# Optimization experiments

Measured on AMD Instinct MI355X. Metric: run time of the kernel, lower is better.

Reference implementation:

```python
import jax, jax.numpy as jnp
import numpy as np

N, E, F, H, O = 50000, 800000, 256, 128, 64


def setup_inputs() -> dict:
    key = jax.random.key(0)
    ks = jax.random.split(key, 8)
    x = jax.random.normal(ks[0], (N, F), jnp.float32)
    edge_index = jax.random.randint(ks[1], (2, E), 0, N, jnp.int32)
    batch = jnp.zeros((N,), jnp.int32)  # single graph
    s = 0.05
    W0 = jax.random.normal(ks[2], (F, H), jnp.float32) * s
    W1 = jax.random.normal(ks[3], (H, H), jnp.float32) * s
    W2 = jax.random.normal(ks[4], (H, H), jnp.float32) * s
    Wlin = jax.random.normal(ks[5], (H, O), jnp.float32) * s
    b0 = jnp.zeros((H,), jnp.float32)
    b1 = jnp.zeros((H,), jnp.float32)
    b2 = jnp.zeros((H,), jnp.float32)
    blin = jnp.zeros((O,), jnp.float32)
    return {"x": x, "edge_index": edge_index, "batch": batch,
            "W0": W0, "b0": b0, "W1": W1, "b1": b1, "W2": W2, "b2": b2,
            "Wlin": Wlin, "blin": blin}


def _gcn_norm(edge_index, n, dtype):
    # GCNConv: add self-loops, symmetric normalization D^-1/2 (A+I) D^-1/2
    loop = jnp.arange(n, dtype=edge_index.dtype)
    src = jnp.concatenate([edge_index[0], loop])
    dst = jnp.concatenate([edge_index[1], loop])
    deg = jax.ops.segment_sum(jnp.ones_like(dst, dtype=dtype), dst, num_segments=n)
    dinv = jnp.where(deg > 0, jax.lax.rsqrt(deg), 0.0)
    norm = dinv[src] * dinv[dst]  # [E+N]
    return src, dst, norm


def _gcn_conv(h, src, dst, norm, b, n):
    # gather-transform-scatter: message = norm * h[src], aggregate at dst
    msg = h[src] * norm[:, None]
    return jax.ops.segment_sum(msg, dst, num_segments=n) + b


def reference(x, edge_index, batch, W0, b0, W1, b1, W2, b2, Wlin, blin):
    n = x.shape[0]
    src, dst, norm = _gcn_norm(edge_index, n, x.dtype)
    h = _gcn_conv(x @ W0, src, dst, norm, b0, n)   # no inter-layer activation in source
    h = _gcn_conv(h @ W1, src, dst, norm, b1, n)
    h = _gcn_conv(h @ W2, src, dst, norm, b2, n)
    # dropout p=0.2 is identity in eval mode
    h = h @ Wlin + blin
    out = jax.ops.segment_max(h, batch, num_segments=1)  # global_max_pool, single graph
    return out
```

## Files before the change

kernel.cpp:

```cpp
#include <hip/hip_runtime.h>
#include <math.h>


typedef __attribute__((ext_vector_type(8))) _Float16 f16x8;
typedef __attribute__((ext_vector_type(4))) _Float16 f16x4;
typedef __attribute__((ext_vector_type(4))) float f32x4;

__device__ __forceinline__ unsigned enc_f32(float f) {
    unsigned u = __float_as_uint(f);
    return (u & 0x80000000u) ? ~u : (u | 0x80000000u);
}
__device__ __forceinline__ float dec_f32(unsigned e) {
    return (e & 0x80000000u) ? __uint_as_float(e & 0x7fffffffu)
                             : __uint_as_float(~e);
}
#define ENC_NEG_INF 0x007FFFFFu

__global__ __launch_bounds__(256) void k_hist(const int* __restrict__ dst,
                                              int* __restrict__ T,
                                              int E, int NB, int chunk) {
    __shared__ int hist[512];
    for (int i = threadIdx.x; i < 512; i += 256) hist[i] = 0;
    __syncthreads();
    const int lo = blockIdx.x * chunk, hi = min(E, lo + chunk);
    for (int e = lo + threadIdx.x; e < hi; e += 256)
        atomicAdd(&hist[dst[e] >> 7], 1);
    __syncthreads();
    for (int b = threadIdx.x; b < NB; b += 256)
        T[b * 256 + blockIdx.x] = hist[b];
}

__global__ __launch_bounds__(1024) void k_scan1(const int* __restrict__ in,
                                                int* __restrict__ excl,
                                                int* __restrict__ bsums, int L) {
    __shared__ int sh[1024];
    int t = threadIdx.x;
    int i = blockIdx.x * 1024 + t;
    int v = (i < L) ? in[i] : 0;
    sh[t] = v;
    __syncthreads();
    for (int off = 1; off < 1024; off <<= 1) {
        int tv = (t >= off) ? sh[t - off] : 0;
        __syncthreads();
        sh[t] += tv;
        __syncthreads();
    }
    if (i < L) excl[i] = sh[t] - v;
    if (t == 1023) bsums[blockIdx.x] = sh[1023];
}

__global__ __launch_bounds__(1024) void k_scan2(const int* __restrict__ bsums,
                                                int* __restrict__ bofs, int nb) {
    __shared__ int sh[1024];
    int t = threadIdx.x;
    int v = (t < nb) ? bsums[t] : 0;
    sh[t] = v;
    __syncthreads();
    for (int off = 1; off < 1024; off <<= 1) {
        int tv = (t >= off) ? sh[t - off] : 0;
        __syncthreads();
        sh[t] += tv;
        __syncthreads();
    }
    if (t < nb) bofs[t] = sh[t] - v;
}

__global__ void k_scan3(int* __restrict__ arr, const int* __restrict__ bofs, int L) {
    int i = blockIdx.x * blockDim.x + threadIdx.x;
    if (i < L) arr[i] += bofs[i >> 10];
}

#define PBT 4096
__global__ __launch_bounds__(256) void k_part(const int* __restrict__ src,
                                              const int* __restrict__ dst,
                                              const int* __restrict__ T2,
                                              unsigned* __restrict__ eb,
                                              int E, int NB, int chunk) {
    __shared__ int hist[512], lexc[512], pos[512], wpos[512];
    __shared__ unsigned sorted[PBT];
    const int t = threadIdx.x;
    const int blk = blockIdx.x;
    const int lo = blk * chunk, hi = min(E, lo + chunk);
    for (int i = t; i < NB; i += 256) wpos[i] = T2[i * 256 + blk];
    __syncthreads();
    for (int tlo = lo; tlo < hi; tlo += PBT) {
        const int thi = min(hi, tlo + PBT);
        const int sz = thi - tlo;
        for (int i = t; i < 512; i += 256) hist[i] = 0;
        __syncthreads();
        for (int e = tlo + t; e < thi; e += 256)
            atomicAdd(&hist[dst[e] >> 7], 1);
        __syncthreads();
        const int i0 = t, i1 = t + 256;
        const int o0 = hist[i0], o1 = hist[i1];
        for (int off = 1; off < 512; off <<= 1) {
            int v0 = (i0 >= off) ? hist[i0 - off] : 0;
            int v1 = (i1 >= off) ? hist[i1 - off] : 0;
            __syncthreads();
            hist[i0] += v0;
            hist[i1] += v1;
            __syncthreads();
        }
        lexc[i0] = hist[i0] - o0; pos[i0] = hist[i0] - o0;
        lexc[i1] = hist[i1] - o1; pos[i1] = hist[i1] - o1;
        __syncthreads();
        for (int e = tlo + t; e < thi; e += 256) {
            int d = dst[e];
            int p = atomicAdd(&pos[d >> 7], 1);
            sorted[p] = ((unsigned)d << 16) | (unsigned)src[e];
        }
        __syncthreads();
        for (int i = t; i < sz; i += 256) {
            unsigned x = sorted[i];
            int b = (int)(x >> 23);
            eb[wpos[b] + (i - lexc[b])] = x;
        }
        __syncthreads();
        wpos[i0] += o0;
        wpos[i1] += o1;
        __syncthreads();
    }
}

#define PCT 6144
__global__ __launch_bounds__(256) void k_build(const unsigned* __restrict__ eb,
                                               const int* __restrict__ T2,
                                               unsigned short* __restrict__ csr,
                                               int* __restrict__ rofs,
                                               float* __restrict__ dinv,
                                               int N, int E, int NB) {
    __shared__ int hist[128], lofs[128], pos[128];
    __shared__ unsigned short ssrc[PCT];
    const int t = threadIdx.x;
    const int b = blockIdx.x;
    const int glo = T2[b * 256];
    const int ghi = (b + 1 < NB) ? T2[(b + 1) * 256] : E;
    const int sz = ghi - glo;
    if (t < 128) hist[t] = 0;
    __syncthreads();
    for (int i = t; i < sz; i += 256)
        atomicAdd(&hist[(eb[glo + i] >> 16) & 127], 1);
    __syncthreads();
    const int o = (t < 128) ? hist[t] : 0;
    for (int off = 1; off < 128; off <<= 1) {
        int v = (t < 128 && t >= off) ? hist[t - off] : 0;
        __syncthreads();
        if (t < 128) hist[t] += v;
        __syncthreads();
    }
    if (t < 128) {
        int ex = hist[t] - o;
        lofs[t] = ex;
        pos[t] = ex;
        int d = b * 128 + t;
        if (d < N) {
            rofs[d] = glo + ex;
            dinv[d] = rsqrtf((float)(o + 1));
        }
    }
    __syncthreads();
    if (sz <= PCT) {
        for (int i = t; i < sz; i += 256) {
            unsigned x = eb[glo + i];
            int p = atomicAdd(&pos[(x >> 16) & 127], 1);
            ssrc[p] = (unsigned short)(x & 0xFFFFu);
        }
        __syncthreads();
        for (int i = t; i < sz; i += 256) csr[glo + i] = ssrc[i];
    } else {
        for (int i = t; i < sz; i += 256) {
            unsigned x = eb[glo + i];
            int p = atomicAdd(&pos[(x >> 16) & 127], 1);
            csr[glo + p] = (unsigned short)(x & 0xFFFFu);
        }
    }
    if (b == 0 && t == 0) rofs[N] = E;
}

template <int PACK>
__global__ __launch_bounds__(256) void k_mm2(const float* __restrict__ A,
                                             const float* __restrict__ B,
                                             float* __restrict__ C,
                                             _Float16* __restrict__ Wp) {
    __shared__ float Bs[128 * 64];
    __shared__ float As[4 * 128];
    const int tid = threadIdx.x;
    const int r0 = blockIdx.x * 4;
#pragma unroll
    for (int it = 0; it < 8; ++it) {
        int f = tid + it * 256;
        *(float4*)&Bs[f * 4] = *(const float4*)&B[(size_t)f * 4];
    }
    if (tid < 128)
        *(float4*)&As[tid * 4] = *(const float4*)&A[(size_t)r0 * 128 + tid * 4];
    __syncthreads();
    const int n = tid & 63;
    const int rh = tid >> 6;
    float a0 = 0.f, a1 = 0.f, a2 = 0.f, a3 = 0.f;
#pragma unroll
    for (int k = 0; k < 128; k += 4) {
        a0 = fmaf(As[rh * 128 + k + 0], Bs[(k + 0) * 64 + n], a0);
        a1 = fmaf(As[rh * 128 + k + 1], Bs[(k + 1) * 64 + n], a1);
        a2 = fmaf(As[rh * 128 + k + 2], Bs[(k + 2) * 64 + n], a2);
        a3 = fmaf(As[rh * 128 + k + 3], Bs[(k + 3) * 64 + n], a3);
    }
    float acc = (a0 + a1) + (a2 + a3);
    const int kk = r0 + rh;
    if (PACK) {
        int j = kk & 7;
        int l = ((kk >> 3) & 3) * 16 + (n & 15);
        int q = kk >> 5;
        int c = n >> 4;
        Wp[((size_t)(c * 8 + q) * 64 + l) * 8 + j] = (_Float16)acc;
    } else {
        C[(size_t)kk * 64 + n] = acc;
    }
}

__global__ __launch_bounds__(256) void k_cvec(const float* __restrict__ b0,
                                              const float* __restrict__ b1,
                                              const float* __restrict__ b2,
                                              const float* __restrict__ blin,
                                              const float* __restrict__ P,
                                              const float* __restrict__ Q,
                                              const float* __restrict__ Wl,
                                              float* __restrict__ cv) {
    __shared__ int nzf;
    if (threadIdx.x == 0) nzf = 0;
    __syncthreads();
    const int v = threadIdx.x >> 6;
    const int n = threadIdx.x & 63;
    if (v < 3) {
        const float* bb = (v == 0) ? b0 : (v == 1) ? b1 : b2;
        const float* M = (v == 0) ? P : (v == 1) ? Q : Wl;
        float a0 = 0.f, a1 = 0.f, a2 = 0.f, a3 = 0.f;
#pragma unroll
        for (int k = 0; k < 128; k += 4) {
            a0 = fmaf(bb[k + 0], M[(k + 0) * 64 + n], a0);
            a1 = fmaf(bb[k + 1], M[(k + 1) * 64 + n], a1);
            a2 = fmaf(bb[k + 2], M[(k + 2) * 64 + n], a2);
            a3 = fmaf(bb[k + 3], M[(k + 3) * 64 + n], a3);
        }
        float c = (a0 + a1) + (a2 + a3);
        if (v == 2) c += blin[n];
        cv[v * 64 + n] = c;
        if (v < 2 && c != 0.f) atomicOr(&nzf, 1);
    }
    __syncthreads();
    if (threadIdx.x == 0) cv[192] = nzf ? 1.f : 0.f;
}

__global__ __launch_bounds__(256) void k_u1(const float* __restrict__ dinv,
                                            const int* __restrict__ rofs,
                                            const unsigned short* __restrict__ csr,
                                            const float* __restrict__ cv,
                                            float* __restrict__ u1,
                                            float* __restrict__ w1, int N) {
    int d = blockIdx.x * 256 + threadIdx.x;
    if (d >= N) return;
    if (cv[192] == 0.f) { u1[d] = 0.f; w1[d] = 0.f; return; }
    float s = 0.f;
    const int beg = rofs[d], end = rofs[d + 1];
    for (int e = beg; e < end; ++e) s += dinv[csr[e]];
    float di = dinv[d];
    float u = di * (s + di);
    u1[d] = u;
    w1[d] = di * u;
}

__global__ __launch_bounds__(256) void k_u2(const float* __restrict__ dinv,
                                            const int* __restrict__ rofs,
                                            const unsigned short* __restrict__ csr,
                                            const float* __restrict__ cv,
                                            const float* __restrict__ w1,
                                            float* __restrict__ u2, int N) {
    int d = blockIdx.x * 256 + threadIdx.x;
    if (d >= N) return;
    if (cv[192] == 0.f) { u2[d] = 0.f; return; }
    float s = 0.f;
    const int beg = rofs[d], end = rofs[d + 1];
    for (int e = beg; e < end; ++e) s += w1[csr[e]];
    u2[d] = dinv[d] * (s + w1[d]);
}

template <int K, int M>
__global__ __launch_bounds__(256, 4) void k_gemm(const void* __restrict__ Av,
                                                 const _Float16* __restrict__ Wp,
                                                 const float* __restrict__ sc,
                                                 _Float16* __restrict__ out,
                                                 int N) {
    constexpr int KB = (K > 128) ? 128 : K;
    constexpr int NQ = K / KB;
    constexpr int NK = KB / 32;
    constexpr int KG = KB / 8;
    constexpr int CT = M / 32;
    constexpr int RT = 3;
    __shared__ _Float16 As[96 * KB];
    const int tid = threadIdx.x;
    const int lane = tid & 63;
    const int wave = tid >> 6;
    const int wrow = wave >> 1;
    const int wcol = wave & 1;
    const int R0 = blockIdx.x * 96;

    f32x4 acc[RT][CT];
#pragma unroll
    for (int rt = 0; rt < RT; ++rt)
#pragma unroll
        for (int ct = 0; ct < CT; ++ct) acc[rt][ct] = (f32x4){0.f, 0.f, 0.f, 0.f};

    for (int q = 0; q < NQ; ++q) {
        if (q) __syncthreads();
        {
            const float* A = (const float*)Av;
#pragma unroll
            for (int it = 0; it < (96 * KB) / (4 * 256); ++it) {
                int idx = tid + it * 256;
                int r = idx >> 5;
                int f4 = idx & 31;
                float4 g = {0.f, 0.f, 0.f, 0.f};
                if (R0 + r < N) g = *(const float4*)&A[(size_t)(R0 + r) * K + q * KB + f4 * 4];
                int kg = f4 >> 1, sub = f4 & 1;
                f16x4 h;
                h[0] = (_Float16)g.x; h[1] = (_Float16)g.y;
                h[2] = (_Float16)g.z; h[3] = (_Float16)g.w;
                *(f16x4*)&As[(r >> 4) * (KG * 128) + kg * 128 + (((r & 15) ^ kg) * 8) + sub * 4] = h;
            }
        }
        __syncthreads();
#pragma unroll
        for (int qq = 0; qq < NK; ++qq) {
            const int kk = q * NK + qq;
            const int kgq = qq * 4 + (lane >> 4);
            f16x8 af[RT], bf[CT];
#pragma unroll
            for (int ct = 0; ct < CT; ++ct) {
                int t = wcol * CT + ct;
                bf[ct] = *(const f16x8*)&Wp[((size_t)(t * (K / 32) + kk) * 64 + lane) * 8];
            }
#pragma unroll
            for (int rt = 0; rt < RT; ++rt) {
                int tr = wrow * RT + rt;
                af[rt] = *(const f16x8*)&As[tr * (KG * 128) + kgq * 128 + (((lane & 15) ^ kgq) * 8)];
            }
#pragma unroll
            for (int rt = 0; rt < RT; ++rt)
#pragma unroll
                for (int ct = 0; ct < CT; ++ct)
                    acc[rt][ct] = __builtin_amdgcn_mfma_f32_16x16x32_f16(af[rt], bf[ct], acc[rt][ct], 0, 0, 0);
        }
    }

    const int quad = lane >> 4;
#pragma unroll
    for (int rt = 0; rt < RT; ++rt)
#pragma unroll
        for (int reg = 0; reg < 4; ++reg) {
            int r = R0 + wrow * 48 + rt * 16 + quad * 4 + reg;
            if (r < N) {
                float s = sc[r];
#pragma unroll
                for (int ct = 0; ct < CT; ++ct) {
                    int c = wcol * (CT * 16) + ct * 16 + (lane & 15);
                    out[(size_t)r * M + c] = (_Float16)(acc[rt][ct][reg] * s);
                }
            }
        }
}

template <int FIN>
__global__ __launch_bounds__(256) void k_agg64(const _Float16* __restrict__ tmp,
                                               const float* __restrict__ dinv,
                                               const int* __restrict__ rofs,
                                               const unsigned short* __restrict__ csr,
                                               const float* __restrict__ u1,
                                               const float* __restrict__ u2,
                                               const float* __restrict__ cv,
                                               _Float16* __restrict__ out,
                                               float* __restrict__ bmax, int N) {
    __shared__ unsigned smax[64];
    const int tid = threadIdx.x;
    const int lane = tid & 63;
    const int wave = tid >> 6;
    const int d = blockIdx.x * 4 + wave;
    const int eh = lane >> 3;
    const int fl = lane & 7;
    if (FIN) {
        if (tid < 64) smax[tid] = ENC_NEG_INF;
        __syncthreads();
    }
    if (d < N) {
        const int beg = rofs[d], end = rofs[d + 1];
        float a[8];
#pragma unroll
        for (int j = 0; j < 8; ++j) a[j] = 0.f;
        f16x8 vd;
        if (eh == 7) vd = *(const f16x8*)&tmp[(size_t)d * 64 + fl * 8];
        for (int base = beg; base < end; base += 32) {
            f16x8 v[4];
            unsigned msk = 0;
#pragma unroll
            for (int i = 0; i < 4; ++i) {
                int idx = base + 8 * i + eh;
                if (idx < end) {
                    int s = csr[idx];
                    v[i] = *(const f16x8*)&tmp[(size_t)s * 64 + fl * 8];
                    msk |= 1u << i;
                }
            }
#pragma unroll
            for (int i = 0; i < 4; ++i)
                if (msk & (1u << i)) {
#pragma unroll
                    for (int j = 0; j < 8; ++j) a[j] += (float)v[i][j];
                }
        }
        if (eh == 7) {
#pragma unroll
            for (int j = 0; j < 8; ++j) a[j] += (float)vd[j];
        }
#pragma unroll
        for (int j = 0; j < 8; ++j) {
            a[j] += __shfl_xor(a[j], 8, 64);
            a[j] += __shfl_xor(a[j], 16, 64);
            a[j] += __shfl_xor(a[j], 32, 64);
        }
        if (FIN == 0) {
            if (eh == 0) {
                float di = dinv[d];
                float s2 = di * di;
                f16x8 o;
#pragma unroll
                for (int j = 0; j < 8; ++j) o[j] = (_Float16)(a[j] * s2);
                *(f16x8*)&out[(size_t)d * 64 + fl * 8] = o;
            }
        } else {
            if (eh == 0) {
                float di = dinv[d];
                float v1 = u1[d], v2 = u2[d];
#pragma unroll
                for (int j = 0; j < 8; ++j) {
                    int f = fl * 8 + j;
                    float z = fmaf(di, a[j],
                              fmaf(v2, cv[f], fmaf(v1, cv[64 + f], cv[128 + f])));
                    atomicMax(&smax[f], enc_f32(z));
                }
            }
        }
    }
    if (FIN) {
        __syncthreads();
        if (tid < 64) bmax[(size_t)blockIdx.x * 64 + tid] = dec_f32(smax[tid]);
    }
}

__global__ __launch_bounds__(256) void k_pool(const float* __restrict__ bmax,
                                              float* __restrict__ out, int nb) {
    __shared__ float sm[4];
    const int f = blockIdx.x;
    float m = -INFINITY;
    for (int b = threadIdx.x; b < nb; b += 256)
        m = fmaxf(m, bmax[(size_t)b * 64 + f]);
#pragma unroll
    for (int off = 1; off < 64; off <<= 1) m = fmaxf(m, __shfl_xor(m, off, 64));
    if ((threadIdx.x & 63) == 0) sm[threadIdx.x >> 6] = m;
    __syncthreads();
    if (threadIdx.x == 0)
        out[f] = fmaxf(fmaxf(sm[0], sm[1]), fmaxf(sm[2], sm[3]));
}

extern "C" void kernel_launch(void* const* d_in, const int* in_sizes, int n_in,
                              void* d_out, int out_size, void* d_ws, size_t ws_size,
                              hipStream_t stream) {
    const float* x    = (const float*)d_in[0];
    const int*   ei   = (const int*)d_in[1];
    const float* W0   = (const float*)d_in[3];
    const float* b0   = (const float*)d_in[4];
    const float* W1   = (const float*)d_in[5];
    const float* b1   = (const float*)d_in[6];
    const float* W2   = (const float*)d_in[7];
    const float* b2   = (const float*)d_in[8];
    const float* Wlin = (const float*)d_in[9];
    const float* blin = (const float*)d_in[10];
    float* out = (float*)d_out;

    const int N = in_sizes[2];
    const int E = in_sizes[1] / 2;
    const int* src = ei;
    const int* dst = ei + E;

    size_t off = 0;
    auto carve = [&](size_t bytes) {
        void* p = (char*)d_ws + off;
        off += (bytes + 255) & ~(size_t)255;
        return p;
    };
    const int NB    = (N + 127) / 128;
    const int L     = NB * 256;
    const int chunk = (E + 255) / 256;
    const int nbAg  = (N + 3) / 4;

    float*          dinv = (float*)carve((size_t)N * 4);
    int*            rofs = (int*)carve((size_t)(N + 1) * 4);
    int*            T    = (int*)carve((size_t)L * 4);
    int*            T2   = (int*)carve((size_t)L * 4);
    int*            bsums = (int*)carve(1024 * 4);
    int*            bofs  = (int*)carve(1024 * 4);
    unsigned*       eb   = (unsigned*)carve((size_t)E * 4);
    unsigned short* csr  = (unsigned short*)carve((size_t)E * 2);
    _Float16*       tmpY = (_Float16*)carve((size_t)N * 64 * 2);
    _Float16*       tmpZ = (_Float16*)carve((size_t)N * 64 * 2);
    float*          u1   = (float*)carve((size_t)N * 4);
    float*          w1   = (float*)carve((size_t)N * 4);
    float*          u2   = (float*)carve((size_t)N * 4);
    float*          bmax = (float*)carve((size_t)nbAg * 64 * 4);
    float*          Q    = (float*)carve(128 * 64 * 4);
    float*          P    = (float*)carve(128 * 64 * 4);
    float*          cv   = (float*)carve(256 * 4);
    _Float16*       wp   = (_Float16*)carve(256 * 64 * 2);
    (void)ws_size; (void)n_in; (void)out_size;

    const int nbG = (N + 95) / 96;
    const int nbS = (L + 1023) / 1024;

    k_mm2<0><<<32, 256, 0, stream>>>(W2, Wlin, Q, nullptr);
    k_mm2<0><<<32, 256, 0, stream>>>(W1, Q, P, nullptr);
    k_mm2<1><<<64, 256, 0, stream>>>(W0, P, nullptr, wp);
    k_cvec<<<1, 256, 0, stream>>>(b0, b1, b2, blin, P, Q, Wlin, cv);

    k_hist<<<256, 256, 0, stream>>>(dst, T, E, NB, chunk);
    k_scan1<<<nbS, 1024, 0, stream>>>(T, T2, bsums, L);
    k_scan2<<<1, 1024, 0, stream>>>(bsums, bofs, nbS);
    k_scan3<<<(L + 255) / 256, 256, 0, stream>>>(T2, bofs, L);
    k_part<<<256, 256, 0, stream>>>(src, dst, T2, eb, E, NB, chunk);
    k_build<<<NB, 256, 0, stream>>>(eb, T2, csr, rofs, dinv, N, E, NB);

    k_u1<<<(N + 255) / 256, 256, 0, stream>>>(dinv, rofs, csr, cv, u1, w1, N);
    k_u2<<<(N + 255) / 256, 256, 0, stream>>>(dinv, rofs, csr, cv, w1, u2, N);

    k_gemm<256, 64><<<nbG, 256, 0, stream>>>(x, wp, dinv, tmpY, N);
    k_agg64<0><<<nbAg, 256, 0, stream>>>(tmpY, dinv, rofs, csr,
                                         nullptr, nullptr, nullptr, tmpZ, nullptr, N);
    k_agg64<0><<<nbAg, 256, 0, stream>>>(tmpZ, dinv, rofs, csr,
                                         nullptr, nullptr, nullptr, tmpY, nullptr, N);
    k_agg64<1><<<nbAg, 256, 0, stream>>>(tmpY, dinv, rofs, csr,
                                         u1, u2, cv, nullptr, bmax, N);
    k_pool<<<64, 256, 0, stream>>>(bmax, out, nbAg);
}
```

Baseline: 265.5 us.

## Merge small setup kernels into fewer launches via block-index dispatch

Several tiny kernels are packed into shared launches that dispatch on block index. The weight-chain products run alongside the dst histogram, the final packed weight product and bias vector run alongside edge partitioning, and the u1/u2 degree-weight passes become extra blocks of the first two aggregation launches. The scan's second and third passes are merged into one kernel in which each block reduces the preceding block sums itself. The goal is to cut launch count and serial dependencies, at the cost of larger shared-memory footprints and a reassociated weight product (W0·W1 first, then by Q).

```diff
diff --git a/kernel.cpp b/kernel.cpp
--- a/kernel.cpp
+++ b/kernel.cpp
@@ -16,18 +16,79 @@
 }
 #define ENC_NEG_INF 0x007FFFFFu
 
-__global__ __launch_bounds__(256) void k_hist(const int* __restrict__ dst,
-                                              int* __restrict__ T,
-                                              int E, int NB, int chunk) {
+__device__ __forceinline__ void mm2v_dev(const float* __restrict__ A,
+                                         const float* __restrict__ B,
+                                         int ldb, int bcol0,
+                                         float* __restrict__ C,
+                                         int ldc, int ccol0,
+                                         _Float16* __restrict__ Wp, int pack,
+                                         int vb, int tid,
+                                         float* __restrict__ Bs,
+                                         float* __restrict__ As) {
+    const int r0 = vb * 4;
+#pragma unroll
+    for (int it = 0; it < 8; ++it) {
+        int f = tid + it * 256;
+        int row = f >> 4, c4 = (f & 15) * 4;
+        *(float4*)&Bs[row * 64 + c4] = *(const float4*)&B[(size_t)row * ldb + bcol0 + c4];
+    }
+    if (tid < 128)
+        *(float4*)&As[tid * 4] = *(const float4*)&A[(size_t)r0 * 128 + tid * 4];
+    __syncthreads();
+    const int n = tid & 63;
+    const int rh = tid >> 6;
+    float a0 = 0.f, a1 = 0.f, a2 = 0.f, a3 = 0.f;
+#pragma unroll
+    for (int k = 0; k < 128; k += 4) {
+        a0 = fmaf(As[rh * 128 + k + 0], Bs[(k + 0) * 64 + n], a0);
+        a1 = fmaf(As[rh * 128 + k + 1], Bs[(k + 1) * 64 + n], a1);
+        a2 = fmaf(As[rh * 128 + k + 2], Bs[(k + 2) * 64 + n], a2);
+        a3 = fmaf(As[rh * 128 + k + 3], Bs[(k + 3) * 64 + n], a3);
+    }
+    float acc = (a0 + a1) + (a2 + a3);
+    const int kk = r0 + rh;
+    if (pack) {
+        int j = kk & 7;
+        int l = ((kk >> 3) & 3) * 16 + (n & 15);
+        int q = kk >> 5;
+        int c = n >> 4;
+        Wp[((size_t)(c * 8 + q) * 64 + l) * 8 + j] = (_Float16)acc;
+    } else {
+        C[(size_t)kk * ldc + ccol0 + n] = acc;
+    }
+}
+
+__global__ __launch_bounds__(256) void kA(const float* __restrict__ W0,
+                                          const float* __restrict__ W1,
+                                          const float* __restrict__ W2,
+                                          const float* __restrict__ Wl,
+                                          const int* __restrict__ dst,
+                                          int* __restrict__ T,
+                                          float* __restrict__ W01,
+                                          float* __restrict__ Q,
+                                          int E, int NB, int chunk) {
+    __shared__ float Bs[128 * 64];
+    __shared__ float As[4 * 128];
     __shared__ int hist[512];
-    for (int i = threadIdx.x; i < 512; i += 256) hist[i] = 0;
-    __syncthreads();
-    const int lo = blockIdx.x * chunk, hi = min(E, lo + chunk);
-    for (int e = lo + threadIdx.x; e < hi; e += 256)
-        atomicAdd(&hist[dst[e] >> 7], 1);
-    __syncthreads();
-    for (int b = threadIdx.x; b < NB; b += 256)
-        T[b * 256 + blockIdx.x] = hist[b];
+    const int b = blockIdx.x;
+    const int tid = threadIdx.x;
+    if (b < 64) {
+        mm2v_dev(W0, W1, 128, 0, W01, 128, 0, nullptr, 0, b, tid, Bs, As);
+    } else if (b < 128) {
+        mm2v_dev(W0, W1, 128, 64, W01, 128, 64, nullptr, 0, b - 64, tid, Bs, As);
+    } else if (b < 160) {
+        mm2v_dev(W2, Wl, 64, 0, Q, 64, 0, nullptr, 0, b - 128, tid, Bs, As);
+    } else {
+        const int blk = b - 160;
+        for (int i = tid; i < 512; i += 256) hist[i] = 0;
+        __syncthreads();
+        const int lo = blk * chunk, hi = min(E, lo + chunk);
+        for (int e = lo + tid; e < hi; e += 256)
+            atomicAdd(&hist[dst[e] >> 7], 1);
+        __syncthreads();
+        for (int bk = tid; bk < NB; bk += 256)
+            T[bk * 256 + blk] = hist[bk];
+    }
 }
 
 __global__ __launch_bounds__(1024) void k_scan1(const int* __restrict__ in,
@@ -49,76 +110,119 @@
     if (t == 1023) bsums[blockIdx.x] = sh[1023];
 }
 
-__global__ __launch_bounds__(1024) void k_scan2(const int* __restrict__ bsums,
-                                                int* __restrict__ bofs, int nb) {
+__global__ __launch_bounds__(1024) void k_scan23(int* __restrict__ excl,
+                                                 const int* __restrict__ bsums,
+                                                 int L) {
     __shared__ int sh[1024];
-    int t = threadIdx.x;
-    int v = (t < nb) ? bsums[t] : 0;
-    sh[t] = v;
-    __syncthreads();
-    for (int off = 1; off < 1024; off <<= 1) {
-        int tv = (t >= off) ? sh[t - off] : 0;
-        __syncthreads();
-        sh[t] += tv;
-        __syncthreads();
-    }
-    if (t < nb) bofs[t] = sh[t] - v;
-}
-
-__global__ void k_scan3(int* __restrict__ arr, const int* __restrict__ bofs, int L) {
-    int i = blockIdx.x * blockDim.x + threadIdx.x;
-    if (i < L) arr[i] += bofs[i >> 10];
+    const int t = threadIdx.x;
+    sh[t] = (t < (int)blockIdx.x) ? bsums[t] : 0;
+    __syncthreads();
+    for (int off = 512; off > 0; off >>= 1) {
+        if (t < off) sh[t] += sh[t + off];
+        __syncthreads();
+    }
+    const int ofs = sh[0];
+    int i = blockIdx.x * 1024 + t;
+    if (i < L) excl[i] += ofs;
 }
 
 #define PBT 4096
-__global__ __launch_bounds__(256) void k_part(const int* __restrict__ src,
-                                              const int* __restrict__ dst,
-                                              const int* __restrict__ T2,
-                                              unsigned* __restrict__ eb,
-                                              int E, int NB, int chunk) {
+__global__ __launch_bounds__(256) void kP(const int* __restrict__ src,
+                                          const int* __restrict__ dst,
+                                          const int* __restrict__ T2,
+                                          unsigned* __restrict__ eb,
+                                          int E, int NB, int chunk,
+                                          const float* __restrict__ W01,
+                                          const float* __restrict__ Q,
+                                          const float* __restrict__ W1,
+                                          const float* __restrict__ b0,
+                                          const float* __restrict__ b1,
+                                          const float* __restrict__ b2,
+                                          const float* __restrict__ blin,
+                                          const float* __restrict__ Wl,
+                                          _Float16* __restrict__ wp,
+                                          float* __restrict__ cv) {
     __shared__ int hist[512], lexc[512], pos[512], wpos[512];
     __shared__ unsigned sorted[PBT];
+    __shared__ float Bs[128 * 64];
+    __shared__ float As[4 * 128];
+    __shared__ float t0s[128];
+    __shared__ int nzf;
     const int t = threadIdx.x;
-    const int blk = blockIdx.x;
-    const int lo = blk * chunk, hi = min(E, lo + chunk);
-    for (int i = t; i < NB; i += 256) wpos[i] = T2[i * 256 + blk];
-    __syncthreads();
-    for (int tlo = lo; tlo < hi; tlo += PBT) {
-        const int thi = min(hi, tlo + PBT);
-        const int sz = thi - tlo;
-        for (int i = t; i < 512; i += 256) hist[i] = 0;
-        __syncthreads();
-        for (int e = tlo + t; e < thi; e += 256)
-            atomicAdd(&hist[dst[e] >> 7], 1);
-        __syncthreads();
-        const int i0 = t, i1 = t + 256;
-        const int o0 = hist[i0], o1 = hist[i1];
-        for (int off = 1; off < 512; off <<= 1) {
-            int v0 = (i0 >= off) ? hist[i0 - off] : 0;
-            int v1 = (i1 >= off) ? hist[i1 - off] : 0;
+    const int b = blockIdx.x;
+    if (b < 256) {
+        const int blk = b;
+        const int lo = blk * chunk, hi = min(E, lo + chunk);
+        for (int i = t; i < NB; i += 256) wpos[i] = T2[i * 256 + blk];
+        __syncthreads();
+        for (int tlo = lo; tlo < hi; tlo += PBT) {
+            const int thi = min(hi, tlo + PBT);
+            const int sz = thi - tlo;
+            for (int i = t; i < 512; i += 256) hist[i] = 0;
             __syncthreads();
-            hist[i0] += v0;
-            hist[i1] += v1;
+            for (int e = tlo + t; e < thi; e += 256)
+                atomicAdd(&hist[dst[e] >> 7], 1);
             __syncthreads();
-        }
-        lexc[i0] = hist[i0] - o0; pos[i0] = hist[i0] - o0;
-        lexc[i1] = hist[i1] - o1; pos[i1] = hist[i1] - o1;
-        __syncthreads();
-        for (int e = tlo + t; e < thi; e += 256) {
-            int d = dst[e];
-            int p = atomicAdd(&pos[d >> 7], 1);
-            sorted[p] = ((unsigned)d << 16) | (unsigned)src[e];
-        }
-        __syncthreads();
-        for (int i = t; i < sz; i += 256) {
-            unsigned x = sorted[i];
-            int b = (int)(x >> 23);
-            eb[wpos[b] + (i - lexc[b])] = x;
-        }
-        __syncthreads();
-        wpos[i0] += o0;
-        wpos[i1] += o1;
-        __syncthreads();
+            const int i0 = t, i1 = t + 256;
+            const int o0 = hist[i0], o1 = hist[i1];
+            for (int off = 1; off < 512; off <<= 1) {
+                int v0 = (i0 >= off) ? hist[i0 - off] : 0;
+                int v1 = (i1 >= off) ? hist[i1 - off] : 0;
+                __syncthreads();
+                hist[i0] += v0;
+                hist[i1] += v1;
+                __syncthreads();
+            }
+            lexc[i0] = hist[i0] - o0; pos[i0] = hist[i0] - o0;
+            lexc[i1] = hist[i1] - o1; pos[i1] = hist[i1] - o1;
+            __syncthreads();
+            for (int e = tlo + t; e < thi; e += 256) {
+                int d = dst[e];
+                int p = atomicAdd(&pos[d >> 7], 1);
+                sorted[p] = ((unsigned)d << 16) | (unsigned)src[e];
+            }
+            __syncthreads();
+            for (int i = t; i < sz; i += 256) {
+                unsigned x = sorted[i];
+                int bb = (int)(x >> 23);
+                eb[wpos[bb] + (i - lexc[bb])] = x;
+            }
+            __syncthreads();
+            wpos[i0] += o0;
+            wpos[i1] += o1;
+            __syncthreads();
+        }
+    } else if (b < 320) {
+        mm2v_dev(W01, Q, 64, 0, nullptr, 0, 0, wp, 1, b - 256, t, Bs, As);
+    } else {
+        if (t == 0) nzf = 0;
+        if (t < 128) {
+            float s = 0.f;
+            for (int j = 0; j < 128; ++j)
+                s = fmaf(b0[j], W1[(size_t)j * 128 + t], s);
+            t0s[t] = s;
+        }
+        __syncthreads();
+        const int v = t >> 6;
+        const int n = t & 63;
+        if (v < 3) {
+            float a0 = 0.f, a1 = 0.f, a2 = 0.f, a3 = 0.f;
+            const float* bb = (v == 0) ? t0s : (v == 1) ? b1 : b2;
+            const float* M = (v == 2) ? Wl : Q;
+#pragma unroll
+            for (int k = 0; k < 128; k += 4) {
+                a0 = fmaf(bb[k + 0], M[(k + 0) * 64 + n], a0);
+                a1 = fmaf(bb[k + 1], M[(k + 1) * 64 + n], a1);
+                a2 = fmaf(bb[k + 2], M[(k + 2) * 64 + n], a2);
+                a3 = fmaf(bb[k + 3], M[(k + 3) * 64 + n], a3);
+            }
+            float c = (a0 + a1) + (a2 + a3);
+            if (v == 2) c += blin[n];
+            cv[v * 64 + n] = c;
+            if (v < 2 && c != 0.f) atomicOr(&nzf, 1);
+        }
+        __syncthreads();
+        if (t == 0) cv[192] = nzf ? 1.f : 0.f;
     }
 }
 
@@ -175,112 +279,6 @@
         }
     }
     if (b == 0 && t == 0) rofs[N] = E;
-}
-
-template <int PACK>
-__global__ __launch_bounds__(256) void k_mm2(const float* __restrict__ A,
-                                             const float* __restrict__ B,
-                                             float* __restrict__ C,
-                                             _Float16* __restrict__ Wp) {
-    __shared__ float Bs[128 * 64];
-    __shared__ float As[4 * 128];
-    const int tid = threadIdx.x;
-    const int r0 = blockIdx.x * 4;
-#pragma unroll
-    for (int it = 0; it < 8; ++it) {
-        int f = tid + it * 256;
-        *(float4*)&Bs[f * 4] = *(const float4*)&B[(size_t)f * 4];
-    }
-    if (tid < 128)
-        *(float4*)&As[tid * 4] = *(const float4*)&A[(size_t)r0 * 128 + tid * 4];
-    __syncthreads();
-    const int n = tid & 63;
-    const int rh = tid >> 6;
-    float a0 = 0.f, a1 = 0.f, a2 = 0.f, a3 = 0.f;
-#pragma unroll
-    for (int k = 0; k < 128; k += 4) {
-        a0 = fmaf(As[rh * 128 + k + 0], Bs[(k + 0) * 64 + n], a0);
-        a1 = fmaf(As[rh * 128 + k + 1], Bs[(k + 1) * 64 + n], a1);
-        a2 = fmaf(As[rh * 128 + k + 2], Bs[(k + 2) * 64 + n], a2);
-        a3 = fmaf(As[rh * 128 + k + 3], Bs[(k + 3) * 64 + n], a3);
-    }
-    float acc = (a0 + a1) + (a2 + a3);
-    const int kk = r0 + rh;
-    if (PACK) {
-        int j = kk & 7;
-        int l = ((kk >> 3) & 3) * 16 + (n & 15);
-        int q = kk >> 5;
-        int c = n >> 4;
-        Wp[((size_t)(c * 8 + q) * 64 + l) * 8 + j] = (_Float16)acc;
-    } else {
-        C[(size_t)kk * 64 + n] = acc;
-    }
-}
-
-__global__ __launch_bounds__(256) void k_cvec(const float* __restrict__ b0,
-                                              const float* __restrict__ b1,
-                                              const float* __restrict__ b2,
-                                              const float* __restrict__ blin,
-                                              const float* __restrict__ P,
-                                              const float* __restrict__ Q,
-                                              const float* __restrict__ Wl,
-                                              float* __restrict__ cv) {
-    __shared__ int nzf;
-    if (threadIdx.x == 0) nzf = 0;
-    __syncthreads();
-    const int v = threadIdx.x >> 6;
-    const int n = threadIdx.x & 63;
-    if (v < 3) {
-        const float* bb = (v == 0) ? b0 : (v == 1) ? b1 : b2;
-        const float* M = (v == 0) ? P : (v == 1) ? Q : Wl;
-        float a0 = 0.f, a1 = 0.f, a2 = 0.f, a3 = 0.f;
-#pragma unroll
-        for (int k = 0; k < 128; k += 4) {
-            a0 = fmaf(bb[k + 0], M[(k + 0) * 64 + n], a0);
-            a1 = fmaf(bb[k + 1], M[(k + 1) * 64 + n], a1);
-            a2 = fmaf(bb[k + 2], M[(k + 2) * 64 + n], a2);
-            a3 = fmaf(bb[k + 3], M[(k + 3) * 64 + n], a3);
-        }
-        float c = (a0 + a1) + (a2 + a3);
-        if (v == 2) c += blin[n];
-        cv[v * 64 + n] = c;
-        if (v < 2 && c != 0.f) atomicOr(&nzf, 1);
-    }
-    __syncthreads();
-    if (threadIdx.x == 0) cv[192] = nzf ? 1.f : 0.f;
-}
-
-__global__ __launch_bounds__(256) void k_u1(const float* __restrict__ dinv,
-                                            const int* __restrict__ rofs,
-                                            const unsigned short* __restrict__ csr,
-                                            const float* __restrict__ cv,
-                                            float* __restrict__ u1,
-                                            float* __restrict__ w1, int N) {
-    int d = blockIdx.x * 256 + threadIdx.x;
-    if (d >= N) return;
-    if (cv[192] == 0.f) { u1[d] = 0.f; w1[d] = 0.f; return; }
-    float s = 0.f;
-    const int beg = rofs[d], end = rofs[d + 1];
-    for (int e = beg; e < end; ++e) s += dinv[csr[e]];
-    float di = dinv[d];
-    float u = di * (s + di);
-    u1[d] = u;
-    w1[d] = di * u;
-}
-
-__global__ __launch_bounds__(256) void k_u2(const float* __restrict__ dinv,
-                                            const int* __restrict__ rofs,
-                                            const unsigned short* __restrict__ csr,
-                                            const float* __restrict__ cv,
-                                            const float* __restrict__ w1,
-                                            float* __restrict__ u2, int N) {
-    int d = blockIdx.x * 256 + threadIdx.x;
-    if (d >= N) return;
-    if (cv[192] == 0.f) { u2[d] = 0.f; return; }
-    float s = 0.f;
-    const int beg = rofs[d], end = rofs[d + 1];
-    for (int e = beg; e < end; ++e) s += w1[csr[e]];
-    u2[d] = dinv[d] * (s + w1[d]);
 }
 
 template <int K, int M>
@@ -368,21 +366,45 @@
         }
 }
 
-template <int FIN>
+template <int FIN, int UP>
 __global__ __launch_bounds__(256) void k_agg64(const _Float16* __restrict__ tmp,
                                                const float* __restrict__ dinv,
                                                const int* __restrict__ rofs,
                                                const unsigned short* __restrict__ csr,
-                                               const float* __restrict__ u1,
-                                               const float* __restrict__ u2,
                                                const float* __restrict__ cv,
+                                               float* __restrict__ u1,
+                                               float* __restrict__ w1,
+                                               float* __restrict__ u2,
                                                _Float16* __restrict__ out,
                                                float* __restrict__ bmax, int N) {
     __shared__ unsigned smax[64];
     const int tid = threadIdx.x;
+    const int nbAg = (N + 3) / 4;
+    const int vb = blockIdx.x;
+    if (UP && vb >= nbAg) {
+        int d = (vb - nbAg) * 256 + tid;
+        if (d >= N) return;
+        if (UP == 1) {
+            if (cv[192] == 0.f) { u1[d] = 0.f; w1[d] = 0.f; return; }
+            float s = 0.f;
+            const int beg = rofs[d], end = rofs[d + 1];
+            for (int e = beg; e < end; ++e) s += dinv[csr[e]];
+            float di = dinv[d];
+            float u = di * (s + di);
+            u1[d] = u;
+            w1[d] = di * u;
+        } else {
+            if (cv[192] == 0.f) { u2[d] = 0.f; return; }
+            float s = 0.f;
+            const int beg = rofs[d], end = rofs[d + 1];
+            for (int e = beg; e < end; ++e) s += w1[csr[e]];
+            u2[d] = dinv[d] * (s + w1[d]);
+        }
+        return;
+    }
     const int lane = tid & 63;
     const int wave = tid >> 6;
-    const int d = blockIdx.x * 4 + wave;
+    const int d = vb * 4 + wave;
     const int eh = lane >> 3;
     const int fl = lane & 7;
     if (FIN) {
@@ -499,13 +521,13 @@
     const int L     = NB * 256;
     const int chunk = (E + 255) / 256;
     const int nbAg  = (N + 3) / 4;
+    const int nbU   = (N + 255) / 256;
 
     float*          dinv = (float*)carve((size_t)N * 4);
     int*            rofs = (int*)carve((size_t)(N + 1) * 4);
     int*            T    = (int*)carve((size_t)L * 4);
     int*            T2   = (int*)carve((size_t)L * 4);
     int*            bsums = (int*)carve(1024 * 4);
-    int*            bofs  = (int*)carve(1024 * 4);
     unsigned*       eb   = (unsigned*)carve((size_t)E * 4);
     unsigned short* csr  = (unsigned short*)carve((size_t)E * 2);
     _Float16*       tmpY = (_Float16*)carve((size_t)N * 64 * 2);
@@ -515,7 +537,7 @@
     float*          u2   = (float*)carve((size_t)N * 4);
     float*          bmax = (float*)carve((size_t)nbAg * 64 * 4);
     float*          Q    = (float*)carve(128 * 64 * 4);
-    float*          P    = (float*)carve(128 * 64 * 4);
+    float*          W01  = (float*)carve(256 * 128 * 4);
     float*          cv   = (float*)carve(256 * 4);
     _Float16*       wp   = (_Float16*)carve(256 * 64 * 2);
     (void)ws_size; (void)n_in; (void)out_size;
@@ -523,27 +545,18 @@
     const int nbG = (N + 95) / 96;
     const int nbS = (L + 1023) / 1024;
 
-    k_mm2<0><<<32, 256, 0, stream>>>(W2, Wlin, Q, nullptr);
-    k_mm2<0><<<32, 256, 0, stream>>>(W1, Q, P, nullptr);
-    k_mm2<1><<<64, 256, 0, stream>>>(W0, P, nullptr, wp);
-    k_cvec<<<1, 256, 0, stream>>>(b0, b1, b2, blin, P, Q, Wlin, cv);
-
-    k_hist<<<256, 256, 0, stream>>>(dst, T, E, NB, chunk);
+    kA<<<416, 256, 0, stream>>>(W0, W1, W2, Wlin, dst, T, W01, Q, E, NB, chunk);
     k_scan1<<<nbS, 1024, 0, stream>>>(T, T2, bsums, L);
-    k_scan2<<<1, 1024, 0, stream>>>(bsums, bofs, nbS);
-    k_scan3<<<(L + 255) / 256, 256, 0, stream>>>(T2, bofs, L);
-    k_part<<<256, 256, 0, stream>>>(src, dst, T2, eb, E, NB, chunk);
+    k_scan23<<<nbS, 1024, 0, stream>>>(T2, bsums, L);
+    kP<<<321, 256, 0, stream>>>(src, dst, T2, eb, E, NB, chunk,
+                                W01, Q, W1, b0, b1, b2, blin, Wlin, wp, cv);
     k_build<<<NB, 256, 0, stream>>>(eb, T2, csr, rofs, dinv, N, E, NB);
-
-    k_u1<<<(N + 255) / 256, 256, 0, stream>>>(dinv, rofs, csr, cv, u1, w1, N);
-    k_u2<<<(N + 255) / 256, 256, 0, stream>>>(dinv, rofs, csr, cv, w1, u2, N);
-
     k_gemm<256, 64><<<nbG, 256, 0, stream>>>(x, wp, dinv, tmpY, N);
-    k_agg64<0><<<nbAg, 256, 0, stream>>>(tmpY, dinv, rofs, csr,
-                                         nullptr, nullptr, nullptr, tmpZ, nullptr, N);
-    k_agg64<0><<<nbAg, 256, 0, stream>>>(tmpZ, dinv, rofs, csr,
-                                         nullptr, nullptr, nullptr, tmpY, nullptr, N);
-    k_agg64<1><<<nbAg, 256, 0, stream>>>(tmpY, dinv, rofs, csr,
-                                         u1, u2, cv, nullptr, bmax, N);
+    k_agg64<0, 1><<<nbAg + nbU, 256, 0, stream>>>(tmpY, dinv, rofs, csr, cv,
+                                                  u1, w1, u2, tmpZ, nullptr, N);
+    k_agg64<0, 2><<<nbAg + nbU, 256, 0, stream>>>(tmpZ, dinv, rofs, csr, cv,
+                                                  u1, w1, u2, tmpY, nullptr, N);
+    k_agg64<1, 0><<<nbAg, 256, 0, stream>>>(tmpY, dinv, rofs, csr, cv,
+                                            u1, w1, u2, nullptr, bmax, N);
     k_pool<<<64, 256, 0, stream>>>(bmax, out, nbAg);
 }
```

Result: faster. 246.1 us (-7.3%).
